# Kernel optimization log

Measured on AMD Instinct MI355X. Metric: run time of the kernel, lower is better.

## Reference

```python
import jax, jax.numpy as jnp
import numpy as np

N, F_IN, HEADS, D_HEAD, HID, OUT, E = 50000, 128, 4, 64, 256, 2, 800000
NEG_SLOPE = 0.2


def setup_inputs() -> dict:
    key = jax.random.key(0)
    ks = jax.random.split(key, 12)
    x = jax.random.normal(ks[0], (N, F_IN), dtype=jnp.float32)
    edge_index = jax.random.randint(ks[1], (2, E), 0, N, dtype=jnp.int64)
    s = 0.05
    W_gat = jax.random.normal(ks[2], (F_IN, HEADS * D_HEAD), dtype=jnp.float32) * s
    att_src = jax.random.normal(ks[3], (HEADS, D_HEAD), dtype=jnp.float32) * s
    att_dst = jax.random.normal(ks[4], (HEADS, D_HEAD), dtype=jnp.float32) * s
    b_gat = jnp.zeros((HEADS * D_HEAD,), dtype=jnp.float32)
    W1 = jax.random.normal(ks[5], (HEADS * D_HEAD, HID), dtype=jnp.float32) * s
    b1 = jnp.zeros((HID,), dtype=jnp.float32)
    W2 = jax.random.normal(ks[6], (HID, HID), dtype=jnp.float32) * s
    b2 = jnp.zeros((HID,), dtype=jnp.float32)
    W3 = jax.random.normal(ks[7], (HID, OUT), dtype=jnp.float32) * s
    b3 = jnp.zeros((OUT,), dtype=jnp.float32)
    return {"x": x, "edge_index": edge_index, "W_gat": W_gat, "att_src": att_src,
            "att_dst": att_dst, "b_gat": b_gat, "W1": W1, "b1": b1,
            "W2": W2, "b2": b2, "W3": W3, "b3": b3}


def _gat(x, edge_index, W_gat, att_src, att_dst, b_gat):
    n = x.shape[0]
    loop = jnp.arange(n, dtype=edge_index.dtype)
    src = jnp.concatenate([edge_index[0], loop])  # [E+N] message sources j
    dst = jnp.concatenate([edge_index[1], loop])  # [E+N] message targets i
    h = (x @ W_gat).reshape(n, HEADS, D_HEAD)      # [N,H,D]
    a_s = jnp.einsum('nhd,hd->nh', h, att_src)     # [N,H]
    a_d = jnp.einsum('nhd,hd->nh', h, att_dst)     # [N,H]
    e = a_s[src] + a_d[dst]                        # [E',H]
    e = jax.nn.leaky_relu(e, NEG_SLOPE)
    # per-destination-node softmax over incoming edges (numerically stable)
    emax = jax.ops.segment_max(e, dst, num_segments=n)
    e = jnp.exp(e - emax[dst])
    denom = jax.ops.segment_sum(e, dst, num_segments=n)
    alpha = e / denom[dst]                         # [E',H]
    msg = h[src] * alpha[:, :, None]               # [E',H,D]
    out = jax.ops.segment_sum(msg, dst, num_segments=n)  # [N,H,D]
    return out.reshape(n, HEADS * D_HEAD) + b_gat


def reference(x, edge_index, W_gat, att_src, att_dst, b_gat, W1, b1, W2, b2, W3, b3):
    h = _gat(x, edge_index, W_gat, att_src, att_dst, b_gat)
    h = jax.nn.relu(h @ W1 + b1)
    h = jax.nn.relu(h @ W2 + b2)
    return h @ W3 + b3
```

## Files before the change

kernel.cpp:

```cpp
#include <hip/hip_runtime.h>
#include <math.h>

#define N_NODES 50000
#define NP 50048
#define F_IN 128
#define HD 256
#define HID 256
#define NE 800000
#define CAP 64
#define NEG_SLOPE 0.2f

#define FILL_BLOCKS (NE / 256)
#define G1_BLOCKS (NP / 32)

typedef __attribute__((ext_vector_type(8))) __bf16 bf16x8;
typedef __attribute__((ext_vector_type(4))) __bf16 bf16x4;
typedef __attribute__((ext_vector_type(4))) float f32x4;

#define GLD_LDS16(g, l)                                                      \
    __builtin_amdgcn_global_load_lds(                                        \
        (const __attribute__((address_space(1))) unsigned int*)(g),          \
        (__attribute__((address_space(3))) unsigned int*)(l), 16, 0, 0)

__device__ __forceinline__ void tile_transpose(const float* __restrict__ W,
                                               __bf16* __restrict__ Wt,
                                               int K, int M, int k0, int m0, int t) {
    __shared__ float tile[64][65];
#pragma unroll
    for (int i = 0; i < 4; ++i) {
        int row = i * 16 + (t >> 4);
        int col = (t & 15) * 4;
        float4 v = *(const float4*)&W[(size_t)(k0 + row) * M + m0 + col];
        tile[row][col] = v.x; tile[row][col + 1] = v.y;
        tile[row][col + 2] = v.z; tile[row][col + 3] = v.w;
    }
    __syncthreads();
#pragma unroll
    for (int i = 0; i < 4; ++i) {
        int mrow = i * 16 + (t >> 4);
        int kcol = (t & 15) * 4;
        bf16x4 o = {(__bf16)tile[kcol][mrow], (__bf16)tile[kcol + 1][mrow],
                    (__bf16)tile[kcol + 2][mrow], (__bf16)tile[kcol + 3][mrow]};
        *(bf16x4*)&Wt[(size_t)(m0 + mrow) * K + k0 + kcol] = o;
    }
}

#define PB_INIT 196
#define PB_WG 8
#define PB_W1 16
#define PB_W2 16

__global__ __launch_bounds__(256) void prep_kernel(const float* __restrict__ Wg,
                                                   const float* __restrict__ W1,
                                                   const float* __restrict__ W2,
                                                   __bf16* __restrict__ Wg_t,
                                                   __bf16* __restrict__ W1_t,
                                                   __bf16* __restrict__ W2_t,
                                                   int* __restrict__ cnt,
                                                   unsigned short* __restrict__ bucket) {
    int b = blockIdx.x, t = threadIdx.x;
    if (b < PB_INIT) {
        int n = b * 256 + t;
        if (n < N_NODES) { cnt[n] = 1; bucket[n * CAP] = (unsigned short)n; }
    } else if (b < PB_INIT + PB_WG) {
        int tt = b - PB_INIT;
        tile_transpose(Wg, Wg_t, F_IN, HD, (tt >> 2) * 64, (tt & 3) * 64, t);
    } else if (b < PB_INIT + PB_WG + PB_W1) {
        int tt = b - PB_INIT - PB_WG;
        tile_transpose(W1, W1_t, HD, HID, (tt >> 2) * 64, (tt & 3) * 64, t);
    } else {
        int tt = b - PB_INIT - PB_WG - PB_W1;
        tile_transpose(W2, W2_t, HID, HID, (tt >> 2) * 64, (tt & 3) * 64, t);
    }
}

__global__ __launch_bounds__(256, 6) void g1_fill_kernel(const float* __restrict__ x,
                                                         const __bf16* __restrict__ Bt,
                                                         const float* __restrict__ att_src,
                                                         const float* __restrict__ att_dst,
                                                         const int* __restrict__ ew,
                                                         __bf16* __restrict__ h,
                                                         float* __restrict__ a_s,
                                                         float* __restrict__ a_d,
                                                         int* __restrict__ cnt,
                                                         unsigned short* __restrict__ bucket) {
    __shared__ __bf16 As[32 * 32];
    __shared__ __bf16 Bs[256 * 32];

    if (blockIdx.x < FILL_BLOCKS) {
        int e = blockIdx.x * 256 + threadIdx.x;
        int hi = ew[2 * e + 1];
        unsigned long long bal = __ballot(hi != 0);
        int src, dst;
        if (bal == 0) { src = ew[2 * e]; dst = ew[2 * NE + 2 * e]; }
        else          { src = ew[e];     dst = ew[NE + e]; }
        int pos = atomicAdd(&cnt[dst], 1);
        if (pos < CAP) bucket[dst * CAP + pos] = (unsigned short)src;
        return;
    }

    const int t = threadIdx.x;
    const int lane = t & 63, wv = t >> 6;
    const int lr = lane & 15, q = lane >> 4, lk = q * 8;
    const int col_off = wv * 64;
    const int row0 = (blockIdx.x - FILL_BLOCKS) * 32;
    const int sr = t >> 3, sk4 = (t & 7) * 4;
    const int sb = t >> 2, skb = (t & 3) * 8;
    const int arow = row0 + sr;
    const bool avalid = arow < N_NODES;

    f32x4 acc[2][4];
#pragma unroll
    for (int r = 0; r < 2; ++r)
#pragma unroll
        for (int c = 0; c < 4; ++c) acc[r][c] = f32x4{0.f, 0.f, 0.f, 0.f};

    for (int k0 = 0; k0 < F_IN; k0 += 32) {
        float4 v = {0, 0, 0, 0};
        if (avalid) v = *(const float4*)&x[(size_t)arow * F_IN + k0 + sk4];
        bf16x4 o = {(__bf16)v.x, (__bf16)v.y, (__bf16)v.z, (__bf16)v.w};
        *(bf16x4*)&As[sr * 32 + sk4] = o;
#pragma unroll
        for (int s = 0; s < 4; ++s) {
            int r = s * 64 + sb;
            GLD_LDS16(&Bt[(size_t)r * F_IN + k0 + skb], &Bs[r * 32 + skb]);
        }
        __syncthreads();
        bf16x8 af[2], bfr[4];
#pragma unroll
        for (int i = 0; i < 2; ++i)
            af[i] = *(const bf16x8*)&As[(i * 16 + lr) * 32 + lk];
#pragma unroll
        for (int c = 0; c < 4; ++c)
            bfr[c] = *(const bf16x8*)&Bs[(col_off + c * 16 + lr) * 32 + lk];
#pragma unroll
        for (int r = 0; r < 2; ++r)
#pragma unroll
            for (int c = 0; c < 4; ++c)
                acc[r][c] = __builtin_amdgcn_mfma_f32_16x16x32_bf16(af[r], bfr[c], acc[r][c], 0, 0, 0);
        __syncthreads();
    }

    float asv[4], adv[4];
#pragma unroll
    for (int c = 0; c < 4; ++c) {
        int col = col_off + c * 16 + lr;
        asv[c] = att_src[col];
        adv[c] = att_dst[col];
    }
    float ps[2][4], pd[2][4];
#pragma unroll
    for (int r = 0; r < 2; ++r)
#pragma unroll
        for (int i = 0; i < 4; ++i) { ps[r][i] = 0.f; pd[r][i] = 0.f; }

#pragma unroll
    for (int c = 0; c < 4; ++c) {
        int col = col_off + c * 16 + lr;
#pragma unroll
        for (int r = 0; r < 2; ++r) {
#pragma unroll
            for (int i = 0; i < 4; ++i) {
                int row = row0 + r * 16 + q * 4 + i;
                float v = acc[r][c][i];
                h[(size_t)row * HD + col] = (__bf16)v;
                ps[r][i] += v * asv[c];
                pd[r][i] += v * adv[c];
            }
        }
    }
#pragma unroll
    for (int r = 0; r < 2; ++r)
#pragma unroll
        for (int i = 0; i < 4; ++i) {
#pragma unroll
            for (int m = 1; m < 16; m <<= 1) {
                ps[r][i] += __shfl_xor(ps[r][i], m);
                pd[r][i] += __shfl_xor(pd[r][i], m);
            }
        }
    if (lr == 0) {
#pragma unroll
        for (int r = 0; r < 2; ++r)
#pragma unroll
            for (int i = 0; i < 4; ++i) {
                int row = row0 + r * 16 + q * 4 + i;
                a_s[row * 4 + wv] = ps[r][i];
                a_d[row * 4 + wv] = pd[r][i];
            }
    }
}

__device__ __forceinline__ float lrelu(float v) { return v >= 0.f ? v : NEG_SLOPE * v; }

__global__ __launch_bounds__(128) void gat_aggregate_kernel(const __bf16* __restrict__ h,
                                                            const float* __restrict__ a_s,
                                                            const float* __restrict__ a_d,
                                                            const int* __restrict__ cnt,
                                                            const unsigned short* __restrict__ bucket,
                                                            const float* __restrict__ b_gat,
                                                            __bf16* __restrict__ gat) {
    __shared__ unsigned short s_src[2][64];
    __shared__ float s_alpha[2][64][4];
    const int lane = threadIdx.x & 63;
    const int wv = threadIdx.x >> 6;
    const int n = blockIdx.x * 2 + wv;

    int deg = cnt[n];
    if (deg > CAP) deg = CAP;
    int src = n;
    float4 e = {-1e30f, -1e30f, -1e30f, -1e30f};
    float4 ad = *(const float4*)&a_d[n * 4];
    if (lane < deg) {
        src = bucket[n * CAP + lane];
        float4 as4 = *(const float4*)&a_s[src * 4];
        e.x = lrelu(as4.x + ad.x);
        e.y = lrelu(as4.y + ad.y);
        e.z = lrelu(as4.z + ad.z);
        e.w = lrelu(as4.w + ad.w);
    }
    float4 m = e;
#pragma unroll
    for (int off = 1; off < 64; off <<= 1) {
        m.x = fmaxf(m.x, __shfl_xor(m.x, off));
        m.y = fmaxf(m.y, __shfl_xor(m.y, off));
        m.z = fmaxf(m.z, __shfl_xor(m.z, off));
        m.w = fmaxf(m.w, __shfl_xor(m.w, off));
    }
    float4 wgt = {0, 0, 0, 0};
    if (lane < deg) {
        wgt.x = __expf(e.x - m.x); wgt.y = __expf(e.y - m.y);
        wgt.z = __expf(e.z - m.z); wgt.w = __expf(e.w - m.w);
    }
    float4 s = wgt;
#pragma unroll
    for (int off = 1; off < 64; off <<= 1) {
        s.x += __shfl_xor(s.x, off); s.y += __shfl_xor(s.y, off);
        s.z += __shfl_xor(s.z, off); s.w += __shfl_xor(s.w, off);
    }
    s_src[wv][lane] = (unsigned short)src;
    s_alpha[wv][lane][0] = wgt.x / s.x;
    s_alpha[wv][lane][1] = wgt.y / s.y;
    s_alpha[wv][lane][2] = wgt.z / s.z;
    s_alpha[wv][lane][3] = wgt.w / s.w;

    const int half = lane >> 5;
    const int l32 = lane & 31;
    const int c0 = l32 * 8;
    const int head = l32 >> 3;
    float acc[8];
#pragma unroll
    for (int k = 0; k < 8; ++k) acc[k] = 0.f;

    const int mde = (deg + 1) & ~1;
    int j = 0;
    for (; j + 8 <= mde; j += 8) {
        int j0 = j + half, j1 = j + 2 + half, j2 = j + 4 + half, j3 = j + 6 + half;
        int s0 = s_src[wv][j0], s1 = s_src[wv][j1];
        int s2 = s_src[wv][j2], s3 = s_src[wv][j3];
        float a0 = s_alpha[wv][j0][head], a1 = s_alpha[wv][j1][head];
        float a2 = s_alpha[wv][j2][head], a3 = s_alpha[wv][j3][head];
        bf16x8 h0 = *(const bf16x8*)&h[(size_t)s0 * HD + c0];
        bf16x8 h1 = *(const bf16x8*)&h[(size_t)s1 * HD + c0];
        bf16x8 h2 = *(const bf16x8*)&h[(size_t)s2 * HD + c0];
        bf16x8 h3 = *(const bf16x8*)&h[(size_t)s3 * HD + c0];
#pragma unroll
        for (int k = 0; k < 8; ++k)
            acc[k] += a0 * (float)h0[k] + a1 * (float)h1[k]
                    + a2 * (float)h2[k] + a3 * (float)h3[k];
    }
    for (; j < mde; j += 2) {
        int j0 = j + half;
        int s0 = s_src[wv][j0];
        float a0 = s_alpha[wv][j0][head];
        bf16x8 h0 = *(const bf16x8*)&h[(size_t)s0 * HD + c0];
#pragma unroll
        for (int k = 0; k < 8; ++k)
            acc[k] += a0 * (float)h0[k];
    }
#pragma unroll
    for (int k = 0; k < 8; ++k) acc[k] += __shfl_xor(acc[k], 32);

    if (half == 0) {
        float4 bg0 = *(const float4*)&b_gat[c0];
        float4 bg1 = *(const float4*)&b_gat[c0 + 4];
        bf16x8 o;
        o[0] = (__bf16)(acc[0] + bg0.x); o[1] = (__bf16)(acc[1] + bg0.y);
        o[2] = (__bf16)(acc[2] + bg0.z); o[3] = (__bf16)(acc[3] + bg0.w);
        o[4] = (__bf16)(acc[4] + bg1.x); o[5] = (__bf16)(acc[5] + bg1.y);
        o[6] = (__bf16)(acc[6] + bg1.z); o[7] = (__bf16)(acc[7] + bg1.w);
        *(bf16x8*)&gat[(size_t)n * HD + c0] = o;
    }
}

__global__ __launch_bounds__(256) void fused_mlp_kernel(const __bf16* __restrict__ A,
                                                        const __bf16* __restrict__ W1t,
                                                        const __bf16* __restrict__ W2t,
                                                        const float* __restrict__ b1,
                                                        const float* __restrict__ b2,
                                                        const float* __restrict__ W3,
                                                        const float* __restrict__ b3,
                                                        float* __restrict__ out) {
    __shared__ __bf16 As[64 * 32];
    __shared__ __bf16 Ws[256 * 32];
    __shared__ __bf16 h1s[8 * 64 * 32];
    __shared__ float s_out[64][2];
    const int t = threadIdx.x;
    const int lane = t & 63, wv = t >> 6;
    const int lr = lane & 15, q = lane >> 4, lk = q * 8;
    const int col_off = wv * 64;
    const int row0 = blockIdx.x * 64;
    const int sr = t >> 2, sk = (t & 3) * 8;

    if (t < 128) ((float*)s_out)[t] = 0.f;

    f32x4 acc[4][4];
#pragma unroll
    for (int r = 0; r < 4; ++r)
#pragma unroll
        for (int c = 0; c < 4; ++c) acc[r][c] = f32x4{0.f, 0.f, 0.f, 0.f};

    for (int k0 = 0; k0 < HD; k0 += 32) {
        GLD_LDS16(&A[(size_t)(row0 + sr) * HD + k0 + sk], &As[sr * 32 + sk]);
#pragma unroll
        for (int s = 0; s < 4; ++s) {
            int r = s * 64 + sr;
            GLD_LDS16(&W1t[(size_t)r * HD + k0 + sk], &Ws[r * 32 + sk]);
        }
        __syncthreads();
        bf16x8 af[4], bfr[4];
#pragma unroll
        for (int i = 0; i < 4; ++i) {
            af[i]  = *(const bf16x8*)&As[(i * 16 + lr) * 32 + lk];
            bfr[i] = *(const bf16x8*)&Ws[(col_off + i * 16 + lr) * 32 + lk];
        }
#pragma unroll
        for (int r = 0; r < 4; ++r)
#pragma unroll
            for (int c = 0; c < 4; ++c)
                acc[r][c] = __builtin_amdgcn_mfma_f32_16x16x32_bf16(af[r], bfr[c], acc[r][c], 0, 0, 0);
        __syncthreads();
    }
#pragma unroll
    for (int c = 0; c < 4; ++c) {
        int col = col_off + c * 16 + lr;
        float bv = b1[col];
        int cb = (col >> 5) * 2048;
        int kk = col & 31;
#pragma unroll
        for (int r = 0; r < 4; ++r)
#pragma unroll
            for (int i = 0; i < 4; ++i) {
                int row = r * 16 + q * 4 + i;
                float v = fmaxf(acc[r][c][i] + bv, 0.f);
                h1s[cb + row * 32 + kk] = (__bf16)v;
                acc[r][c][i] = 0.f;
            }
    }
    __syncthreads();

    for (int k0 = 0; k0 < HID; k0 += 32) {
#pragma unroll
        for (int s = 0; s < 4; ++s) {
            int r = s * 64 + sr;
            GLD_LDS16(&W2t[(size_t)r * HID + k0 + sk], &Ws[r * 32 + sk]);
        }
        __syncthreads();
        const int cb = (k0 >> 5) * 2048;
        bf16x8 af[4], bfr[4];
#pragma unroll
        for (int i = 0; i < 4; ++i) {
            af[i]  = *(const bf16x8*)&h1s[cb + (i * 16 + lr) * 32 + lk];
            bfr[i] = *(const bf16x8*)&Ws[(col_off + i * 16 + lr) * 32 + lk];
        }
#pragma unroll
        for (int r = 0; r < 4; ++r)
#pragma unroll
            for (int c = 0; c < 4; ++c)
                acc[r][c] = __builtin_amdgcn_mfma_f32_16x16x32_bf16(af[r], bfr[c], acc[r][c], 0, 0, 0);
        __syncthreads();
    }

    float b2v[4], w30[4], w31[4];
#pragma unroll
    for (int c = 0; c < 4; ++c) {
        int col = col_off + c * 16 + lr;
        b2v[c] = b2[col];
        w30[c] = W3[col * 2];
        w31[c] = W3[col * 2 + 1];
    }
#pragma unroll
    for (int r = 0; r < 4; ++r) {
#pragma unroll
        for (int i = 0; i < 4; ++i) {
            float o0 = 0.f, o1 = 0.f;
#pragma unroll
            for (int c = 0; c < 4; ++c) {
                float v = fmaxf(acc[r][c][i] + b2v[c], 0.f);
                o0 += v * w30[c];
                o1 += v * w31[c];
            }
#pragma unroll
            for (int m = 1; m < 16; m <<= 1) {
                o0 += __shfl_xor(o0, m);
                o1 += __shfl_xor(o1, m);
            }
            if (lr == 0) {
                int row = r * 16 + q * 4 + i;
                atomicAdd(&s_out[row][0], o0);
                atomicAdd(&s_out[row][1], o1);
            }
        }
    }
    __syncthreads();
    if (t < 128) {
        int row = t >> 1, o = t & 1;
        int g = row0 + row;
        if (g < N_NODES) out[g * 2 + o] = s_out[row][o] + b3[o];
    }
}

extern "C" void kernel_launch(void* const* d_in, const int* in_sizes, int n_in,
                              void* d_out, int out_size, void* d_ws, size_t ws_size,
                              hipStream_t stream) {
    const float* x       = (const float*)d_in[0];
    const int*   ei      = (const int*)d_in[1];
    const float* W_gat   = (const float*)d_in[2];
    const float* att_src = (const float*)d_in[3];
    const float* att_dst = (const float*)d_in[4];
    const float* b_gat   = (const float*)d_in[5];
    const float* W1      = (const float*)d_in[6];
    const float* b1      = (const float*)d_in[7];
    const float* W2      = (const float*)d_in[8];
    const float* b2      = (const float*)d_in[9];
    const float* W3      = (const float*)d_in[10];
    const float* b3      = (const float*)d_in[11];
    float* out = (float*)d_out;

    char* ws = (char*)d_ws;
    __bf16* h_bf   = (__bf16*)ws;  ws += (size_t)NP * HD * 2;
    __bf16* gat_bf = (__bf16*)ws;  ws += (size_t)NP * HD * 2;
    __bf16* Wg_t   = (__bf16*)ws;  ws += (size_t)HD * F_IN * 2;
    __bf16* W1_t   = (__bf16*)ws;  ws += (size_t)HID * HD * 2;
    __bf16* W2_t   = (__bf16*)ws;  ws += (size_t)HID * HID * 2;
    float* a_s     = (float*)ws;   ws += (size_t)NP * 4 * 4;
    float* a_d     = (float*)ws;   ws += (size_t)NP * 4 * 4;
    int* cnt       = (int*)ws;     ws += (size_t)N_NODES * 4;
    unsigned short* bucket = (unsigned short*)ws;
    ws += (size_t)N_NODES * CAP * 2;

    prep_kernel<<<PB_INIT + PB_WG + PB_W1 + PB_W2, 256, 0, stream>>>(
        W_gat, W1, W2, Wg_t, W1_t, W2_t, cnt, bucket);
    g1_fill_kernel<<<FILL_BLOCKS + G1_BLOCKS, 256, 0, stream>>>(
        x, Wg_t, att_src, att_dst, ei, h_bf, a_s, a_d, cnt, bucket);
    gat_aggregate_kernel<<<N_NODES / 2, 128, 0, stream>>>(h_bf, a_s, a_d, cnt, bucket,
                                                          b_gat, gat_bf);
    fused_mlp_kernel<<<NP / 64, 256, 0, stream>>>(gat_bf, W1_t, W2_t, b1, b2, W3, b3, out);
}
```

Baseline: 254.2 us.

## Enlarge GEMM tile to 64 rows, batch edge fill, implicit self-loops

The h = x@W_gat GEMM block grows from 32 to 64 rows, with wider 8-element staging loads and a 4x4 MFMA accumulator per wave. This raises reuse of the shared W tile and halves the number of GEMM blocks. Edge-fill blocks now handle four edges per thread, and those blocks are ordered after the GEMM blocks. Self-loops are no longer written into the bucket; the aggregate kernel adds the self edge implicitly, and a memset replaces the init blocks in the prep kernel. In exchange, register pressure rises (the occupancy hint is removed), the bucket capacity for real edges drops by one, and an extra memset launch is added.

```diff
diff --git a/kernel.cpp b/kernel.cpp
--- a/kernel.cpp
+++ b/kernel.cpp
@@ -10,8 +10,8 @@
 #define CAP 64
 #define NEG_SLOPE 0.2f
 
-#define FILL_BLOCKS (NE / 256)
-#define G1_BLOCKS (NP / 32)
+#define G1_BLOCKS (NP / 64)
+#define FILL_BLOCKS ((NE + 1023) / 1024)
 
 typedef __attribute__((ext_vector_type(8))) __bf16 bf16x8;
 typedef __attribute__((ext_vector_type(4))) __bf16 bf16x4;
@@ -45,7 +45,6 @@
     }
 }
 
-#define PB_INIT 196
 #define PB_WG 8
 #define PB_W1 16
 #define PB_W2 16
@@ -55,47 +54,57 @@
                                                    const float* __restrict__ W2,
                                                    __bf16* __restrict__ Wg_t,
                                                    __bf16* __restrict__ W1_t,
-                                                   __bf16* __restrict__ W2_t,
-                                                   int* __restrict__ cnt,
-                                                   unsigned short* __restrict__ bucket) {
+                                                   __bf16* __restrict__ W2_t) {
     int b = blockIdx.x, t = threadIdx.x;
-    if (b < PB_INIT) {
-        int n = b * 256 + t;
-        if (n < N_NODES) { cnt[n] = 1; bucket[n * CAP] = (unsigned short)n; }
-    } else if (b < PB_INIT + PB_WG) {
-        int tt = b - PB_INIT;
-        tile_transpose(Wg, Wg_t, F_IN, HD, (tt >> 2) * 64, (tt & 3) * 64, t);
-    } else if (b < PB_INIT + PB_WG + PB_W1) {
-        int tt = b - PB_INIT - PB_WG;
+    if (b < PB_WG) {
+        tile_transpose(Wg, Wg_t, F_IN, HD, (b >> 2) * 64, (b & 3) * 64, t);
+    } else if (b < PB_WG + PB_W1) {
+        int tt = b - PB_WG;
         tile_transpose(W1, W1_t, HD, HID, (tt >> 2) * 64, (tt & 3) * 64, t);
     } else {
-        int tt = b - PB_INIT - PB_WG - PB_W1;
+        int tt = b - PB_WG - PB_W1;
         tile_transpose(W2, W2_t, HID, HID, (tt >> 2) * 64, (tt & 3) * 64, t);
     }
 }
 
-__global__ __launch_bounds__(256, 6) void g1_fill_kernel(const float* __restrict__ x,
-                                                         const __bf16* __restrict__ Bt,
-                                                         const float* __restrict__ att_src,
-                                                         const float* __restrict__ att_dst,
-                                                         const int* __restrict__ ew,
-                                                         __bf16* __restrict__ h,
-                                                         float* __restrict__ a_s,
-                                                         float* __restrict__ a_d,
-                                                         int* __restrict__ cnt,
-                                                         unsigned short* __restrict__ bucket) {
-    __shared__ __bf16 As[32 * 32];
+__global__ __launch_bounds__(256) void g1_fill_kernel(const float* __restrict__ x,
+                                                      const __bf16* __restrict__ Bt,
+                                                      const float* __restrict__ att_src,
+                                                      const float* __restrict__ att_dst,
+                                                      const int* __restrict__ ew,
+                                                      __bf16* __restrict__ h,
+                                                      float* __restrict__ a_s,
+                                                      float* __restrict__ a_d,
+                                                      int* __restrict__ cnt,
+                                                      unsigned short* __restrict__ bucket) {
+    __shared__ __bf16 As[64 * 32];
     __shared__ __bf16 Bs[256 * 32];
 
-    if (blockIdx.x < FILL_BLOCKS) {
-        int e = blockIdx.x * 256 + threadIdx.x;
-        int hi = ew[2 * e + 1];
+    if (blockIdx.x >= G1_BLOCKS) {
+        int e0 = (blockIdx.x - G1_BLOCKS) * 1024 + threadIdx.x;
+        int hi = ew[2 * e0 + 1];
         unsigned long long bal = __ballot(hi != 0);
-        int src, dst;
-        if (bal == 0) { src = ew[2 * e]; dst = ew[2 * NE + 2 * e]; }
-        else          { src = ew[e];     dst = ew[NE + e]; }
-        int pos = atomicAdd(&cnt[dst], 1);
-        if (pos < CAP) bucket[dst * CAP + pos] = (unsigned short)src;
+        const bool is64 = (bal == 0);
+        int ee[4], ss[4], dd[4], pos[4];
+        int cnt_local = 0;
+#pragma unroll
+        for (int i = 0; i < 4; ++i) {
+            int e = e0 + i * 256;
+            if (e < NE) {
+                int src, dst;
+                if (is64) { src = ew[2 * e]; dst = ew[2 * NE + 2 * e]; }
+                else      { src = ew[e];     dst = ew[NE + e]; }
+                ee[cnt_local] = e; ss[cnt_local] = src; dd[cnt_local] = dst;
+                ++cnt_local;
+            }
+        }
+#pragma unroll
+        for (int i = 0; i < 4; ++i)
+            if (i < cnt_local) pos[i] = atomicAdd(&cnt[dd[i]], 1);
+#pragma unroll
+        for (int i = 0; i < 4; ++i)
+            if (i < cnt_local && pos[i] < CAP - 1)
+                bucket[dd[i] * CAP + pos[i]] = (unsigned short)ss[i];
         return;
     }
 
@@ -103,38 +112,42 @@
     const int lane = t & 63, wv = t >> 6;
     const int lr = lane & 15, q = lane >> 4, lk = q * 8;
     const int col_off = wv * 64;
-    const int row0 = (blockIdx.x - FILL_BLOCKS) * 32;
-    const int sr = t >> 3, sk4 = (t & 7) * 4;
-    const int sb = t >> 2, skb = (t & 3) * 8;
+    const int row0 = blockIdx.x * 64;
+    const int sr = t >> 2, sk = (t & 3) * 8;
     const int arow = row0 + sr;
     const bool avalid = arow < N_NODES;
 
-    f32x4 acc[2][4];
-#pragma unroll
-    for (int r = 0; r < 2; ++r)
+    f32x4 acc[4][4];
+#pragma unroll
+    for (int r = 0; r < 4; ++r)
 #pragma unroll
         for (int c = 0; c < 4; ++c) acc[r][c] = f32x4{0.f, 0.f, 0.f, 0.f};
 
     for (int k0 = 0; k0 < F_IN; k0 += 32) {
-        float4 v = {0, 0, 0, 0};
-        if (avalid) v = *(const float4*)&x[(size_t)arow * F_IN + k0 + sk4];
-        bf16x4 o = {(__bf16)v.x, (__bf16)v.y, (__bf16)v.z, (__bf16)v.w};
-        *(bf16x4*)&As[sr * 32 + sk4] = o;
+        float4 v0 = {0, 0, 0, 0}, v1 = {0, 0, 0, 0};
+        if (avalid) {
+            const float* xp = &x[(size_t)arow * F_IN + k0 + sk];
+            v0 = *(const float4*)xp;
+            v1 = *(const float4*)(xp + 4);
+        }
+        bf16x8 o;
+        o[0] = (__bf16)v0.x; o[1] = (__bf16)v0.y; o[2] = (__bf16)v0.z; o[3] = (__bf16)v0.w;
+        o[4] = (__bf16)v1.x; o[5] = (__bf16)v1.y; o[6] = (__bf16)v1.z; o[7] = (__bf16)v1.w;
+        *(bf16x8*)&As[sr * 32 + sk] = o;
 #pragma unroll
         for (int s = 0; s < 4; ++s) {
-            int r = s * 64 + sb;
-            GLD_LDS16(&Bt[(size_t)r * F_IN + k0 + skb], &Bs[r * 32 + skb]);
-        }
-        __syncthreads();
-        bf16x8 af[2], bfr[4];
-#pragma unroll
-        for (int i = 0; i < 2; ++i)
-            af[i] = *(const bf16x8*)&As[(i * 16 + lr) * 32 + lk];
-#pragma unroll
-        for (int c = 0; c < 4; ++c)
-            bfr[c] = *(const bf16x8*)&Bs[(col_off + c * 16 + lr) * 32 + lk];
-#pragma unroll
-        for (int r = 0; r < 2; ++r)
+            int r = s * 64 + sr;
+            GLD_LDS16(&Bt[(size_t)r * F_IN + k0 + sk], &Bs[r * 32 + sk]);
+        }
+        __syncthreads();
+        bf16x8 af[4], bfr[4];
+#pragma unroll
+        for (int i = 0; i < 4; ++i) {
+            af[i]  = *(const bf16x8*)&As[(i * 16 + lr) * 32 + lk];
+            bfr[i] = *(const bf16x8*)&Bs[(col_off + i * 16 + lr) * 32 + lk];
+        }
+#pragma unroll
+        for (int r = 0; r < 4; ++r)
 #pragma unroll
             for (int c = 0; c < 4; ++c)
                 acc[r][c] = __builtin_amdgcn_mfma_f32_16x16x32_bf16(af[r], bfr[c], acc[r][c], 0, 0, 0);
@@ -148,9 +161,9 @@
         asv[c] = att_src[col];
         adv[c] = att_dst[col];
     }
-    float ps[2][4], pd[2][4];
-#pragma unroll
-    for (int r = 0; r < 2; ++r)
+    float ps[4][4], pd[4][4];
+#pragma unroll
+    for (int r = 0; r < 4; ++r)
 #pragma unroll
         for (int i = 0; i < 4; ++i) { ps[r][i] = 0.f; pd[r][i] = 0.f; }
 
@@ -158,7 +171,7 @@
     for (int c = 0; c < 4; ++c) {
         int col = col_off + c * 16 + lr;
 #pragma unroll
-        for (int r = 0; r < 2; ++r) {
+        for (int r = 0; r < 4; ++r) {
 #pragma unroll
             for (int i = 0; i < 4; ++i) {
                 int row = row0 + r * 16 + q * 4 + i;
@@ -170,7 +183,7 @@
         }
     }
 #pragma unroll
-    for (int r = 0; r < 2; ++r)
+    for (int r = 0; r < 4; ++r)
 #pragma unroll
         for (int i = 0; i < 4; ++i) {
 #pragma unroll
@@ -181,7 +194,7 @@
         }
     if (lr == 0) {
 #pragma unroll
-        for (int r = 0; r < 2; ++r)
+        for (int r = 0; r < 4; ++r)
 #pragma unroll
             for (int i = 0; i < 4; ++i) {
                 int row = row0 + r * 16 + q * 4 + i;
@@ -206,13 +219,14 @@
     const int wv = threadIdx.x >> 6;
     const int n = blockIdx.x * 2 + wv;
 
-    int deg = cnt[n];
-    if (deg > CAP) deg = CAP;
+    int deg_e = cnt[n];
+    if (deg_e > CAP - 1) deg_e = CAP - 1;
+    const int deg = deg_e + 1;
     int src = n;
     float4 e = {-1e30f, -1e30f, -1e30f, -1e30f};
     float4 ad = *(const float4*)&a_d[n * 4];
     if (lane < deg) {
-        src = bucket[n * CAP + lane];
+        if (lane < deg_e) src = bucket[n * CAP + lane];
         float4 as4 = *(const float4*)&a_s[src * 4];
         e.x = lrelu(as4.x + ad.x);
         e.y = lrelu(as4.y + ad.y);
@@ -449,9 +463,10 @@
     unsigned short* bucket = (unsigned short*)ws;
     ws += (size_t)N_NODES * CAP * 2;
 
-    prep_kernel<<<PB_INIT + PB_WG + PB_W1 + PB_W2, 256, 0, stream>>>(
-        W_gat, W1, W2, Wg_t, W1_t, W2_t, cnt, bucket);
-    g1_fill_kernel<<<FILL_BLOCKS + G1_BLOCKS, 256, 0, stream>>>(
+    hipMemsetAsync(cnt, 0, (size_t)N_NODES * 4, stream);
+    prep_kernel<<<PB_WG + PB_W1 + PB_W2, 256, 0, stream>>>(
+        W_gat, W1, W2, Wg_t, W1_t, W2_t);
+    g1_fill_kernel<<<G1_BLOCKS + FILL_BLOCKS, 256, 0, stream>>>(
         x, Wg_t, att_src, att_dst, ei, h_bf, a_s, a_d, cnt, bucket);
     gat_aggregate_kernel<<<N_NODES / 2, 128, 0, stream>>>(h_bf, a_s, a_d, cnt, bucket,
                                                           b_gat, gat_bf);
```

After: 255.1 us. About the same (+0.3%).
